# Performance work log

Measured on AMD Instinct MI355X. Metric: run time of the kernel, lower is better.

Reference implementation:

```python
import jax, jax.numpy as jnp
import numpy as np

NHEAD = 16


def setup_inputs() -> dict:
    key = jax.random.key(0)
    ks = jax.random.split(key, 9)
    d = 1024
    scale = 0.03  # keep projected q,k in a sane range (like trained weights)
    return {
        "x": jax.random.normal(ks[0], (4, 4096, d), jnp.float32),
        "wq": jax.random.normal(ks[1], (d, d), jnp.float32) * scale,
        "bq": jax.random.normal(ks[2], (d,), jnp.float32) * scale,
        "wk": jax.random.normal(ks[3], (d, d), jnp.float32) * scale,
        "bk": jax.random.normal(ks[4], (d,), jnp.float32) * scale,
        "wv": jax.random.normal(ks[5], (d, d), jnp.float32) * scale,
        "bv": jax.random.normal(ks[6], (d,), jnp.float32) * scale,
        "wo": jax.random.normal(ks[7], (d, d), jnp.float32) * scale,
        "bo": jax.random.normal(ks[8], (d,), jnp.float32) * scale,
        "window_size": 128,
    }


def reference(x, wq, bq, wk, bk, wv, bv, wo, bo, window_size):
    B, S, D = x.shape
    H = NHEAD
    Dh = D // H
    w = int(window_size)

    def proj(wm, b):
        # [B,S,D] -> [B,H,S,Dh]
        return (x @ wm.T + b).reshape(B, S, H, Dh).transpose(0, 2, 1, 3)

    q = proj(wq, bq)
    k = proj(wk, bk)
    v = proj(wv, bv)

    # Pad K/V along seq so offset slices are static-size [B,H,S,Dh].
    Kp = jnp.pad(k, ((0, 0), (0, 0), (w, w), (0, 0)))
    Vp = jnp.pad(v, ((0, 0), (0, 0), (w, w), (0, 0)))
    pos = jnp.arange(S)
    inv_sqrt = np.float32(1.0 / np.sqrt(Dh))

    # Faithful to the Triton kernel: a sequential scan over window offsets with a
    # RUNNING max but NO rescaling of the accumulators (the kernel's exact math).
    def step(carry, t):
        m, o_acc, t_acc = carry
        kj = jax.lax.dynamic_slice_in_dim(Kp, t, S, axis=2)  # key at offset t-w
        vj = jax.lax.dynamic_slice_in_dim(Vp, t, S, axis=2)
        s = jnp.einsum("bhsd,bhsd->bhs", q, kj) * inv_sqrt
        j = pos + t - w
        valid = (j >= 0) & (j < S)  # [S], broadcasts over [B,H,S]
        m_new = jnp.where(valid, jnp.maximum(m, s), m)
        p = jnp.exp(jnp.where(valid, s - m_new, -jnp.inf))  # 0 where invalid
        return (m_new, o_acc + p[..., None] * vj, t_acc + p), None

    init = (
        jnp.full((B, H, S), -jnp.inf, dtype=x.dtype),
        jnp.zeros((B, H, S, Dh), dtype=x.dtype),
        jnp.zeros((B, H, S), dtype=x.dtype),
    )
    (m, o_acc, t_acc), _ = jax.lax.scan(step, init, jnp.arange(2 * w + 1))
    o = o_acc / t_acc[..., None]  # [B,H,S,Dh]
    out = o.transpose(0, 2, 1, 3).reshape(B, S, D)
    return out @ wo.T + bo
```

## Files before the change

kernel.cpp:

```cpp
#include <hip/hip_runtime.h>
#include <math.h>

#define S_LEN  4096
#define BATCH  4
#define DMODEL 1024
#define NHEADS 16
#define DHEAD  64
#define WIN    128

typedef _Float16 half8   __attribute__((ext_vector_type(8)));
typedef _Float16 half4_t __attribute__((ext_vector_type(4)));
typedef float    floatx4 __attribute__((ext_vector_type(4)));

__device__ __forceinline__ void gload16(const void* g, void* l) {
    __builtin_amdgcn_global_load_lds(
        (const __attribute__((address_space(1))) void*)g,
        (__attribute__((address_space(3))) void*)l, 16, 0, 0);
}

__global__ __launch_bounds__(256)
void cvt_f32_f16(const float4* __restrict__ in, half4_t* __restrict__ out, int n4) {
    for (int i = blockIdx.x * blockDim.x + threadIdx.x; i < n4;
         i += gridDim.x * blockDim.x) {
        const float4 a = in[i];
        half4_t h;
        h[0] = (_Float16)a.x; h[1] = (_Float16)a.y;
        h[2] = (_Float16)a.z; h[3] = (_Float16)a.w;
        out[i] = h;
    }
}

__global__ __launch_bounds__(256)
void cvt4_f32_f16(const float4* __restrict__ w0, const float4* __restrict__ w1,
                  const float4* __restrict__ w2, const float4* __restrict__ w3,
                  half4_t* __restrict__ o0, half4_t* __restrict__ o1,
                  half4_t* __restrict__ o2, half4_t* __restrict__ o3, int n4) {
    const float4* in  = blockIdx.y == 0 ? w0 : (blockIdx.y == 1 ? w1 : (blockIdx.y == 2 ? w2 : w3));
    half4_t*      out = blockIdx.y == 0 ? o0 : (blockIdx.y == 1 ? o1 : (blockIdx.y == 2 ? o2 : o3));
    for (int i = blockIdx.x * blockDim.x + threadIdx.x; i < n4;
         i += gridDim.x * blockDim.x) {
        const float4 a = in[i];
        half4_t h;
        h[0] = (_Float16)a.x; h[1] = (_Float16)a.y;
        h[2] = (_Float16)a.z; h[3] = (_Float16)a.w;
        out[i] = h;
    }
}

template<int MODE, int NT>
__global__ __launch_bounds__(256)
void gemm128(const _Float16* __restrict__ A, const _Float16* __restrict__ W,
             const float* __restrict__ B0, const float* __restrict__ B1,
             const float* __restrict__ B2, void* __restrict__ out_base)
{
    const int K = DMODEL;

    const int bid = blockIdx.x;
    const int swz = (bid & 7) * (16 * NT) + (bid >> 3);
    const int i0  = (swz / NT) * 128;
    const int n0  = (swz % NT) * 128;

    __shared__ _Float16 As[128 * 32];
    __shared__ _Float16 Bs[128 * 32];

    const int tid  = threadIdx.x;
    const int lane = tid & 63;
    const int wid  = tid >> 6;
    const int wr   = wid >> 1, wc = wid & 1;

    const int srow = tid >> 2;
    const int scol = (tid & 3) * 8;
    const _Float16* gA0 = A + (size_t)(i0 + srow) * K + scol;
    const _Float16* gA1 = A + (size_t)(i0 + 64 + srow) * K + scol;
    const _Float16* gB0 = W + (size_t)(n0 + srow) * K + scol;
    const _Float16* gB1 = W + (size_t)(n0 + 64 + srow) * K + scol;
    _Float16* lA0 = As + tid * 8;
    _Float16* lA1 = As + 2048 + tid * 8;
    _Float16* lB0 = Bs + tid * 8;
    _Float16* lB1 = Bs + 2048 + tid * 8;

    floatx4 acc[4][4];
    #pragma unroll
    for (int mi = 0; mi < 4; ++mi)
        #pragma unroll
        for (int ni = 0; ni < 4; ++ni) acc[mi][ni] = (floatx4)0.f;

    const int frow = lane & 15;
    const int fk   = (lane >> 4) * 8;
    const int aoff = (wr * 64 + frow) * 32 + fk;
    const int boff = (wc * 64 + frow) * 32 + fk;

    for (int k0 = 0; k0 < K; k0 += 32) {
        gload16(gA0 + k0, lA0);
        gload16(gA1 + k0, lA1);
        gload16(gB0 + k0, lB0);
        gload16(gB1 + k0, lB1);
        __syncthreads();

        half8 a[4], b[4];
        #pragma unroll
        for (int mi = 0; mi < 4; ++mi) a[mi] = *(const half8*)&As[aoff + mi * 512];
        #pragma unroll
        for (int ni = 0; ni < 4; ++ni) b[ni] = *(const half8*)&Bs[boff + ni * 512];
        #pragma unroll
        for (int mi = 0; mi < 4; ++mi)
            #pragma unroll
            for (int ni = 0; ni < 4; ++ni)
                acc[mi][ni] = __builtin_amdgcn_mfma_f32_16x16x32_f16(
                    a[mi], b[ni], acc[mi][ni], 0, 0, 0);
        __syncthreads();
    }

    const int r0 = (lane >> 4) * 4;
    const int cn = lane & 15;
    const int z  = n0 >> 10;
    const float* bz = (MODE == 1) ? B0 : (z == 0 ? B0 : (z == 1 ? B1 : B2));

    #pragma unroll
    for (int ni = 0; ni < 4; ++ni) {
        const int gc   = n0 + wc * 64 + ni * 16 + cn;
        const int gcol = gc & (DMODEL - 1);
        const float bv = bz[gcol];
        #pragma unroll
        for (int mi = 0; mi < 4; ++mi) {
            const int gr = i0 + wr * 64 + mi * 16 + r0;
            const floatx4 v = acc[mi][ni];
            if (MODE == 0) {
                _Float16* outh = (_Float16*)out_base
                               + (size_t)z * ((size_t)16384 * DMODEL);
                const int b  = gr >> 12;
                const int sp = gr & (S_LEN - 1);
                const int h  = gcol >> 6;
                const int dh = gcol & 63;
                if (z < 2) {
                    #pragma unroll
                    for (int r = 0; r < 4; ++r)
                        outh[((((size_t)(b * NHEADS + h)) * S_LEN + sp + r) << 6) + dh] =
                            (_Float16)(v[r] + bv);
                } else {
                    half4_t hv;
                    hv[0] = (_Float16)(v[0] + bv); hv[1] = (_Float16)(v[1] + bv);
                    hv[2] = (_Float16)(v[2] + bv); hv[3] = (_Float16)(v[3] + bv);
                    *(half4_t*)&outh[(((size_t)(b * NHEADS + h)) * DHEAD + dh) * S_LEN + sp] = hv;
                }
            } else {
                float* out = (float*)out_base;
                #pragma unroll
                for (int r = 0; r < 4; ++r)
                    out[(size_t)(gr + r) * DMODEL + gcol] = v[r] + bv;
            }
        }
    }
}

__global__ __launch_bounds__(256)
void attn_mfma(const _Float16* __restrict__ qh_, const _Float16* __restrict__ kh_,
               const _Float16* __restrict__ vth_, _Float16* __restrict__ o)
{
    __shared__ __align__(16) _Float16 Qs[64 * 64];
    __shared__ __align__(16) _Float16 Ks[64 * 64];
    __shared__ __align__(16) _Float16 Vt[64 * 64];
    __shared__ __align__(16) float    SP[64 * 68];
    __shared__ __align__(16) _Float16 P16[64 * 64];
    __shared__ float CM[64 * 4];
    __shared__ float TSs[64 * 4];
    __shared__ float Mq[64];
    __shared__ float Tq[64];

    const int tid   = threadIdx.x;
    const int lane  = tid & 63;
    const int w     = tid >> 6;
    const int qbase = blockIdx.x * 64;
    const int head  = blockIdx.y, b = blockIdx.z;
    const size_t bh = (size_t)(b * NHEADS + head);

    const _Float16* qg = qh_  + bh * (size_t)(S_LEN * DHEAD);
    const _Float16* kg = kh_  + bh * (size_t)(S_LEN * DHEAD);
    const _Float16* vg = vth_ + bh * (size_t)(DHEAD * S_LEN);

    const int fr = lane & 15;
    const int fh = lane >> 4;

    #pragma unroll
    for (int rep = 0; rep < 2; ++rep) {
        const int c = tid + 256 * rep;
        const int row = c >> 3, sl = c & 7;
        gload16(qg + (size_t)(qbase + row) * 64 + (size_t)((sl ^ (row & 7)) * 8),
                Qs + (size_t)c * 8);
    }
    if (tid < 64) { Mq[tid] = -INFINITY; Tq[tid] = 0.f; }

    floatx4 Oacc[4];
    #pragma unroll
    for (int ni = 0; ni < 4; ++ni) Oacc[ni] = (floatx4)0.f;

    for (int c = 0; c < 5; ++c) {
        const int jlo = qbase - WIN + c * 64;
        if (jlo < 0 || jlo >= S_LEN) continue;
        const int base_rel = jlo - qbase + WIN;

        __syncthreads();

        #pragma unroll
        for (int rep = 0; rep < 2; ++rep) {
            const int cc = tid + 256 * rep;
            const int row = cc >> 3, sl = cc & 7;
            gload16(kg + (size_t)(jlo + row) * 64 + (size_t)((sl ^ (row & 7)) * 8),
                    Ks + (size_t)cc * 8);
            gload16(vg + (size_t)row * S_LEN + jlo + (size_t)((sl ^ (row & 7)) * 8),
                    Vt + (size_t)cc * 8);
        }
        __syncthreads();

        {
            floatx4 acc[4];
            #pragma unroll
            for (int ni = 0; ni < 4; ++ni) acc[ni] = (floatx4)0.f;
            half8 a[2];
            #pragma unroll
            for (int kc = 0; kc < 2; ++kc) {
                const int row = 16 * w + fr;
                a[kc] = *(const half8*)&Qs[row * 64 + ((fh + 4 * kc) ^ (row & 7)) * 8];
            }
            #pragma unroll
            for (int ni = 0; ni < 4; ++ni)
                #pragma unroll
                for (int kc = 0; kc < 2; ++kc) {
                    const int tr = 16 * ni + fr;
                    half8 bf = *(const half8*)&Ks[tr * 64 + ((fh + 4 * kc) ^ (tr & 7)) * 8];
                    acc[ni] = __builtin_amdgcn_mfma_f32_16x16x32_f16(a[kc], bf, acc[ni], 0, 0, 0);
                }
            #pragma unroll
            for (int ni = 0; ni < 4; ++ni)
                #pragma unroll
                for (int r = 0; r < 4; ++r)
                    SP[(16 * w + 4 * fh + r) * 68 + fr + 16 * ni] = acc[ni][r] * 0.125f;
        }
        __syncthreads();

        const int sq = lane;
        float sv[16], run[16];
        {
            float m_run = -INFINITY;
            #pragma unroll
            for (int u = 0; u < 4; ++u) {
                const float4 s4 = *(const float4*)&SP[sq * 68 + w * 16 + 4 * u];
                const float se[4] = {s4.x, s4.y, s4.z, s4.w};
                #pragma unroll
                for (int e = 0; e < 4; ++e) {
                    const int i = 4 * u + e;
                    const int rel = base_rel + 16 * w + i - sq;
                    const bool valid = (rel >= 0) && (rel <= 2 * WIN);
                    const float s = valid ? se[e] : -INFINITY;
                    sv[i] = s;
                    m_run = fmaxf(m_run, s);
                    run[i] = m_run;
                }
            }
            CM[sq * 4 + w] = m_run;
        }
        __syncthreads();

        {
            float pre = Mq[sq];
            if (w > 0) pre = fmaxf(pre, CM[sq * 4 + 0]);
            if (w > 1) pre = fmaxf(pre, CM[sq * 4 + 1]);
            if (w > 2) pre = fmaxf(pre, CM[sq * 4 + 2]);
            float tl = 0.f;
            _Float16 pf[16];
            #pragma unroll
            for (int i = 0; i < 16; ++i) {
                const float wv = fmaxf(pre, run[i]);
                const float p = (sv[i] != -INFINITY) ? __expf(sv[i] - wv) : 0.f;
                tl += p;
                pf[i] = (_Float16)p;
            }
            TSs[sq * 4 + w] = tl;
            #pragma unroll
            for (int u = 0; u < 2; ++u) {
                half8 h8;
                #pragma unroll
                for (int e = 0; e < 8; ++e) h8[e] = pf[8 * u + e];
                *(half8*)&P16[sq * 64 + ((2 * w + u) ^ (sq & 7)) * 8] = h8;
            }
        }
        __syncthreads();

        if (tid < 64) {
            const float mm = fmaxf(fmaxf(CM[tid * 4 + 0], CM[tid * 4 + 1]),
                                   fmaxf(CM[tid * 4 + 2], CM[tid * 4 + 3]));
            Mq[tid] = fmaxf(Mq[tid], mm);
            Tq[tid] += TSs[tid * 4 + 0] + TSs[tid * 4 + 1] + TSs[tid * 4 + 2] + TSs[tid * 4 + 3];
        }

        {
            half8 pa[2];
            #pragma unroll
            for (int kc = 0; kc < 2; ++kc) {
                const int row = 16 * w + fr;
                pa[kc] = *(const half8*)&P16[row * 64 + ((fh + 4 * kc) ^ (row & 7)) * 8];
            }
            #pragma unroll
            for (int ni = 0; ni < 4; ++ni)
                #pragma unroll
                for (int kc = 0; kc < 2; ++kc) {
                    const int dr = 16 * ni + fr;
                    half8 bf = *(const half8*)&Vt[dr * 64 + ((fh + 4 * kc) ^ (dr & 7)) * 8];
                    Oacc[ni] = __builtin_amdgcn_mfma_f32_16x16x32_f16(pa[kc], bf, Oacc[ni], 0, 0, 0);
                }
        }
    }

    __syncthreads();

    #pragma unroll
    for (int ni = 0; ni < 4; ++ni)
        #pragma unroll
        for (int r = 0; r < 4; ++r) {
            const int q  = 16 * w + 4 * fh + r;
            const float inv = 1.0f / Tq[q];
            o[((size_t)(b * S_LEN + qbase + q) * NHEADS + head) * DHEAD + fr + 16 * ni] =
                (_Float16)(Oacc[ni][r] * inv);
        }
}

extern "C" void kernel_launch(void* const* d_in, const int* in_sizes, int n_in,
                              void* d_out, int out_size, void* d_ws, size_t ws_size,
                              hipStream_t stream) {
    const float* x  = (const float*)d_in[0];
    const float* wq = (const float*)d_in[1];
    const float* bq = (const float*)d_in[2];
    const float* wk = (const float*)d_in[3];
    const float* bk = (const float*)d_in[4];
    const float* wv = (const float*)d_in[5];
    const float* bv = (const float*)d_in[6];
    const float* wo = (const float*)d_in[7];
    const float* bo = (const float*)d_in[8];

    const size_t BUF = (size_t)BATCH * S_LEN * DMODEL;
    _Float16* xh  = (_Float16*)d_ws;
    _Float16* qh  = xh + BUF;
    _Float16* kh  = qh + BUF;
    _Float16* vth = kh + BUF;
    _Float16* oh  = vth + BUF;
    _Float16* wqh = oh + BUF;
    _Float16* wkh = wqh + DMODEL * DMODEL;
    _Float16* wvh = wkh + DMODEL * DMODEL;
    _Float16* woh = wvh + DMODEL * DMODEL;

    cvt_f32_f16<<<2048, 256, 0, stream>>>((const float4*)x, (half4_t*)xh, (int)(BUF / 4));
    cvt4_f32_f16<<<dim3(256, 4), 256, 0, stream>>>(
        (const float4*)wq, (const float4*)wk, (const float4*)wv, (const float4*)wo,
        (half4_t*)wqh, (half4_t*)wkh, (half4_t*)wvh, (half4_t*)woh,
        DMODEL * DMODEL / 4);

    gemm128<0, 24><<<128 * 24, 256, 0, stream>>>(xh, wqh, bq, bk, bv, (void*)qh);

    dim3 gattn(S_LEN / 64, NHEADS, BATCH);
    attn_mfma<<<gattn, 256, 0, stream>>>(qh, kh, vth, oh);

    gemm128<1, 8><<<128 * 8, 256, 0, stream>>>(oh, woh, bo, bo, bo, d_out);
}
```

Before: 297.6 us.

## Replace 128x128 GEMM with 256x128 tile, 3-stage LDS ring pipeline

Replaces the single-buffered 128x128x32 GEMM with a 512-thread 256x128 tile that uses K-steps of 64 and a three-deep shared-memory ring filled by async global-to-LDS loads. Loads are issued two stages ahead, with vmcnt waits, XOR-swizzled LDS rows and setprio around the MFMA bursts. The aim is to hide global memory latency, cut barrier overhead and raise arithmetic intensity in both the QKV and output projections. The ring uses 144 KB of LDS per block, which limits occupancy to one workgroup per CU, and the 256-row tiles halve the grid size.

```diff
diff --git a/kernel.cpp b/kernel.cpp
--- a/kernel.cpp
+++ b/kernel.cpp
@@ -47,83 +47,118 @@
     }
 }
 
-template<int MODE, int NT>
-__global__ __launch_bounds__(256)
-void gemm128(const _Float16* __restrict__ A, const _Float16* __restrict__ W,
+#define XRS(row) ((((row) >> 2) & 1) << 1)
+
+template<int MODE, int NTN>
+__global__ __launch_bounds__(512)
+void gemm256(const _Float16* __restrict__ A, const _Float16* __restrict__ W,
              const float* __restrict__ B0, const float* __restrict__ B1,
              const float* __restrict__ B2, void* __restrict__ out_base)
 {
     const int K = DMODEL;
-
-    const int bid = blockIdx.x;
-    const int swz = (bid & 7) * (16 * NT) + (bid >> 3);
-    const int i0  = (swz / NT) * 128;
-    const int n0  = (swz % NT) * 128;
-
-    __shared__ _Float16 As[128 * 32];
-    __shared__ _Float16 Bs[128 * 32];
-
-    const int tid  = threadIdx.x;
-    const int lane = tid & 63;
-    const int wid  = tid >> 6;
-    const int wr   = wid >> 1, wc = wid & 1;
-
-    const int srow = tid >> 2;
-    const int scol = (tid & 3) * 8;
-    const _Float16* gA0 = A + (size_t)(i0 + srow) * K + scol;
-    const _Float16* gA1 = A + (size_t)(i0 + 64 + srow) * K + scol;
-    const _Float16* gB0 = W + (size_t)(n0 + srow) * K + scol;
-    const _Float16* gB1 = W + (size_t)(n0 + 64 + srow) * K + scol;
-    _Float16* lA0 = As + tid * 8;
-    _Float16* lA1 = As + 2048 + tid * 8;
-    _Float16* lB0 = Bs + tid * 8;
-    _Float16* lB1 = Bs + 2048 + tid * 8;
-
-    floatx4 acc[4][4];
-    #pragma unroll
-    for (int mi = 0; mi < 4; ++mi)
-        #pragma unroll
-        for (int ni = 0; ni < 4; ++ni) acc[mi][ni] = (floatx4)0.f;
-
-    const int frow = lane & 15;
-    const int fk   = (lane >> 4) * 8;
-    const int aoff = (wr * 64 + frow) * 32 + fk;
-    const int boff = (wc * 64 + frow) * 32 + fk;
-
-    for (int k0 = 0; k0 < K; k0 += 32) {
-        gload16(gA0 + k0, lA0);
-        gload16(gA1 + k0, lA1);
-        gload16(gB0 + k0, lB0);
-        gload16(gB1 + k0, lB1);
-        __syncthreads();
-
-        half8 a[4], b[4];
-        #pragma unroll
-        for (int mi = 0; mi < 4; ++mi) a[mi] = *(const half8*)&As[aoff + mi * 512];
-        #pragma unroll
-        for (int ni = 0; ni < 4; ++ni) b[ni] = *(const half8*)&Bs[boff + ni * 512];
-        #pragma unroll
-        for (int mi = 0; mi < 4; ++mi)
-            #pragma unroll
-            for (int ni = 0; ni < 4; ++ni)
-                acc[mi][ni] = __builtin_amdgcn_mfma_f32_16x16x32_f16(
-                    a[mi], b[ni], acc[mi][ni], 0, 0, 0);
-        __syncthreads();
+    const int bid  = blockIdx.x;
+    const int nwg8 = (NTN * 64) >> 3;
+    const int swz  = (bid & 7) * nwg8 + (bid >> 3);
+    const int i0   = (swz / NTN) * 256;
+    const int n0   = (swz % NTN) * 128;
+
+    __shared__ _Float16 ringA[3][256 * 64];
+    __shared__ _Float16 ringB[3][128 * 64];
+
+    const int tid   = threadIdx.x;
+    const int lane  = tid & 63;
+    const int wid   = tid >> 6;
+    const int wr    = wid >> 2;
+    const int wc    = wid & 3;
+    const int fr    = lane & 15;
+    const int fh    = lane >> 4;
+    const int sl    = tid & 7;
+    const int rbase = tid >> 3;
+
+    floatx4 acc[8][2];
+    #pragma unroll
+    for (int mi = 0; mi < 8; ++mi) {
+        acc[mi][0] = (floatx4)0.f;
+        acc[mi][1] = (floatx4)0.f;
+    }
+
+    auto stageA = [&](int s, int k0) {
+        #pragma unroll
+        for (int r = 0; r < 4; ++r) {
+            const int row = rbase + r * 64;
+            gload16(A + (size_t)(i0 + row) * K + k0 + ((sl ^ XRS(row)) << 3),
+                    &ringA[s][(size_t)tid * 8 + r * 4096]);
+        }
+    };
+    auto stageB = [&](int s, int k0) {
+        #pragma unroll
+        for (int r = 0; r < 2; ++r) {
+            const int row = rbase + r * 64;
+            gload16(W + (size_t)(n0 + row) * K + k0 + ((sl ^ XRS(row)) << 3),
+                    &ringB[s][(size_t)tid * 8 + r * 4096]);
+        }
+    };
+
+    stageA(0, 0);  stageB(0, 0);
+    stageA(1, 64); stageB(1, 64);
+    asm volatile("s_waitcnt vmcnt(6)" ::: "memory");
+    __builtin_amdgcn_s_barrier();
+
+    const int nt = K / 64;
+    int rd = 0;
+    for (int t = 0; t < nt; ++t) {
+        if (t + 2 < nt) {
+            const int st = rd == 0 ? 2 : rd - 1;
+            stageA(st, (t + 2) * 64);
+            stageB(st, (t + 2) * 64);
+        }
+
+        #pragma unroll
+        for (int kc = 0; kc < 2; ++kc) {
+            half8 a[8], b[2];
+            #pragma unroll
+            for (int mi = 0; mi < 8; ++mi) {
+                const int R = wr * 128 + mi * 16 + fr;
+                a[mi] = *(const half8*)&ringA[rd][R * 64 + ((((kc << 2) | fh) ^ XRS(R)) << 3)];
+            }
+            #pragma unroll
+            for (int ni = 0; ni < 2; ++ni) {
+                const int R = wc * 32 + ni * 16 + fr;
+                b[ni] = *(const half8*)&ringB[rd][R * 64 + ((((kc << 2) | fh) ^ XRS(R)) << 3)];
+            }
+            __builtin_amdgcn_s_setprio(1);
+            #pragma unroll
+            for (int mi = 0; mi < 8; ++mi)
+                #pragma unroll
+                for (int ni = 0; ni < 2; ++ni)
+                    acc[mi][ni] = __builtin_amdgcn_mfma_f32_16x16x32_f16(
+                        a[mi], b[ni], acc[mi][ni], 0, 0, 0);
+            __builtin_amdgcn_s_setprio(0);
+        }
+
+        asm volatile("s_waitcnt lgkmcnt(0)" ::: "memory");
+        if (t + 2 < nt) {
+            asm volatile("s_waitcnt vmcnt(6)" ::: "memory");
+        } else if (t + 1 < nt) {
+            asm volatile("s_waitcnt vmcnt(0)" ::: "memory");
+        }
+        if (t + 1 < nt) __builtin_amdgcn_s_barrier();
+        rd = rd + 1 == 3 ? 0 : rd + 1;
     }
 
     const int r0 = (lane >> 4) * 4;
     const int cn = lane & 15;
-    const int z  = n0 >> 10;
+    const int z  = (MODE == 0) ? (n0 >> 10) : 0;
     const float* bz = (MODE == 1) ? B0 : (z == 0 ? B0 : (z == 1 ? B1 : B2));
 
     #pragma unroll
-    for (int ni = 0; ni < 4; ++ni) {
-        const int gc   = n0 + wc * 64 + ni * 16 + cn;
+    for (int ni = 0; ni < 2; ++ni) {
+        const int gc   = n0 + wc * 32 + ni * 16 + cn;
         const int gcol = gc & (DMODEL - 1);
         const float bv = bz[gcol];
         #pragma unroll
-        for (int mi = 0; mi < 4; ++mi) {
-            const int gr = i0 + wr * 64 + mi * 16 + r0;
+        for (int mi = 0; mi < 8; ++mi) {
+            const int gr = i0 + wr * 128 + mi * 16 + r0;
             const floatx4 v = acc[mi][ni];
             if (MODE == 0) {
                 _Float16* outh = (_Float16*)out_base
@@ -184,8 +219,8 @@
     #pragma unroll
     for (int rep = 0; rep < 2; ++rep) {
         const int c = tid + 256 * rep;
-        const int row = c >> 3, sl = c & 7;
-        gload16(qg + (size_t)(qbase + row) * 64 + (size_t)((sl ^ (row & 7)) * 8),
+        const int row = c >> 3, sll = c & 7;
+        gload16(qg + (size_t)(qbase + row) * 64 + (size_t)((sll ^ (row & 7)) * 8),
                 Qs + (size_t)c * 8);
     }
     if (tid < 64) { Mq[tid] = -INFINITY; Tq[tid] = 0.f; }
@@ -204,10 +239,10 @@
         #pragma unroll
         for (int rep = 0; rep < 2; ++rep) {
             const int cc = tid + 256 * rep;
-            const int row = cc >> 3, sl = cc & 7;
-            gload16(kg + (size_t)(jlo + row) * 64 + (size_t)((sl ^ (row & 7)) * 8),
+            const int row = cc >> 3, sll = cc & 7;
+            gload16(kg + (size_t)(jlo + row) * 64 + (size_t)((sll ^ (row & 7)) * 8),
                     Ks + (size_t)cc * 8);
-            gload16(vg + (size_t)row * S_LEN + jlo + (size_t)((sl ^ (row & 7)) * 8),
+            gload16(vg + (size_t)row * S_LEN + jlo + (size_t)((sll ^ (row & 7)) * 8),
                     Vt + (size_t)cc * 8);
         }
         __syncthreads();
@@ -354,10 +389,10 @@
         (half4_t*)wqh, (half4_t*)wkh, (half4_t*)wvh, (half4_t*)woh,
         DMODEL * DMODEL / 4);
 
-    gemm128<0, 24><<<128 * 24, 256, 0, stream>>>(xh, wqh, bq, bk, bv, (void*)qh);
+    gemm256<0, 24><<<64 * 24, 512, 0, stream>>>(xh, wqh, bq, bk, bv, (void*)qh);
 
     dim3 gattn(S_LEN / 64, NHEADS, BATCH);
     attn_mfma<<<gattn, 256, 0, stream>>>(qh, kh, vth, oh);
 
-    gemm128<1, 8><<<128 * 8, 256, 0, stream>>>(oh, woh, bo, bo, bo, d_out);
-}
+    gemm256<1, 8><<<64 * 8, 512, 0, stream>>>(oh, woh, bo, bo, bo, d_out);
+}
```

Measured after the change: 316.6 us. 1.06x slower.
